# Optimization experiments

Hardware: AMD Instinct MI355X
Metric: run time of the kernel (lower is better)

Reference implementation:

```python
import jax, jax.numpy as jnp
import numpy as np
from jax import lax

# channels holding diagonal entries of the embedded 4x4 bA (16:32) and bW (32:48)
_DIAG_CH = np.array([16, 21, 26, 31, 32, 37, 42, 47])
_EPS = 1e-4  # Tikhonov term for per-pixel matrix inversion stability


def _interp_matrix(out_n, in_n):
    """Dense 1D bicubic (a=-0.75) align_corners=True interpolation matrix, torch-compatible."""
    if out_n == in_n:
        return jnp.eye(out_n, dtype=jnp.float32)
    a = -0.75
    scale = (in_n - 1) / (out_n - 1)
    src = np.arange(out_n) * scale
    i0 = np.floor(src).astype(np.int64)
    W = np.zeros((out_n, in_n), np.float64)
    rows = np.arange(out_n)
    for k in range(-1, 3):
        t = np.abs(src - (i0 + k))
        w = np.where(t <= 1.0, (a + 2) * t**3 - (a + 3) * t**2 + 1.0,
                     np.where(t < 2.0, a * t**3 - 5 * a * t**2 + 8 * a * t - 4 * a, 0.0))
        np.add.at(W, (rows, np.clip(i0 + k, 0, in_n - 1)), w)  # border replication
    return jnp.asarray(W, jnp.float32)


def _conv(x, w, b):
    y = lax.conv_general_dilated(x, w, (1, 1), 'SAME',
                                 dimension_numbers=('NCHW', 'OIHW', 'NCHW'))
    return y + b[None, :, None, None]


def _leaky(x):
    return jnp.where(x >= 0, x, 0.01 * x)


def _mm_features(x):
    """compute_mm + intensity: x is (b,48,h,w) -> (b,17,h,w)."""
    b, c, h, w = x.shape
    v = jnp.moveaxis(x, 1, -1)                 # (b,h,w,48)
    F = v[..., :16].reshape(b, h, w, 4, 4)     # intensity frames
    A = v[..., 16:32].reshape(b, h, w, 4, 4)   # analyzer calib bA
    Wm = v[..., 32:48].reshape(b, h, w, 4, 4)  # generator calib bW
    eye = _EPS * jnp.eye(4, dtype=x.dtype)
    M = jnp.linalg.inv(A + eye) @ F @ jnp.linalg.inv(Wm + eye)  # M = A^-1 F W^-1
    inten = v[..., :16].mean(-1)[:, None]      # (b,1,h,w)
    m = jnp.moveaxis(M.reshape(b, h, w, 16), -1, 1)  # (b,16,h,w)
    return jnp.concatenate([inten, m], axis=1)


def _maxpool4(x):
    b, c, h, w = x.shape
    return x.reshape(b, c, h // 4, 4, w // 4, 4).max(axis=(3, 5))


def setup_inputs() -> dict:
    key = jax.random.key(0)
    ks = jax.random.split(key, 6)
    x = 0.3 * jax.random.normal(ks[0], (2, 48, 512, 512), jnp.float32)
    diag = jnp.asarray(_DIAG_CH)
    x = x.at[:, diag].add(1.0)  # well-conditioned per-pixel bA/bW ~ I + noise

    def bias48():
        return jnp.zeros((48,), jnp.float32).at[diag].set(1.0)

    iW0 = 0.05 * jax.random.normal(ks[1], (48, 48, 3, 3), jnp.float32)
    iW1 = 0.05 * jax.random.normal(ks[2], (48, 48, 3, 3), jnp.float32)
    oW0 = 0.05 * jax.random.normal(ks[3], (17, 17, 3, 3), jnp.float32)
    oW1 = 0.05 * jax.random.normal(ks[4], (17, 17, 3, 3), jnp.float32)
    return dict(x=x,
                iW0=iW0, iB0=bias48(), iW1=iW1, iB1=bias48(),
                oW0=oW0, oB0=jnp.zeros((17,), jnp.float32),
                oW1=oW1, oB1=jnp.zeros((17,), jnp.float32))


def reference(x, iW0, iB0, iW1, iB1, oW0, oB0, oW1, oB1):
    b, _, h, w = x.shape
    iparams = [(iW0, iB0), (iW1, iB1)]
    oparams = [(oW0, oB0), (oW1, oB1)]
    outs = []
    for lvl in range(2):  # fixed pyramid levels
        x = _leaky(_conv(x, *iparams[lvl]))
        m = _mm_features(x)                       # (b,17,hl,wl)
        Wh = _interp_matrix(h, m.shape[2])
        Ww = _interp_matrix(w, m.shape[3])
        m = jnp.einsum('Oh,bchw->bcOw', Wh, m)    # bicubic upsample rows
        m = jnp.einsum('Pw,bchw->bchP', Ww, m)    # bicubic upsample cols
        m = _leaky(_conv(m, *oparams[lvl]))
        outs.append(m)
        x = _maxpool4(x)
    return jnp.concatenate(outs, axis=1)          # (b,34,h,w)
```

## Files before the change

### kernel.cpp

```cpp
#include <hip/hip_runtime.h>
#include <math.h>


__device__ __forceinline__ float leakyf(float t) { return t >= 0.0f ? t : 0.01f * t; }

template<int CIN, int OCPT, int PX, int TW, bool DO_POOL, bool TWO_SRC>
__global__ __launch_bounds__(256, 2)
void conv3x3_leaky(const float* __restrict__ in, const float* __restrict__ wgt,
                   const float* __restrict__ bias, float* __restrict__ out,
                   float* __restrict__ pool_out,
                   int H, int W, int COUT, int NG,
                   int in_bstride, int out_bstride, int out_coff,
                   const float* __restrict__ in2, const float* __restrict__ wgt2,
                   const float* __restrict__ bias2, int coff2, int z_split)
{
    constexpr int XG     = TW / PX;
    constexpr int TH     = 256 / XG;
    constexpr int COLS   = TW + 2;
    constexpr int ROWS   = TH + 2;
    constexpr int STRIDE = (COLS + 3) & ~3;
    constexpr int TSZ    = ROWS * STRIDE;
    constexpr int ELEMS  = ROWS * COLS;
    constexpr int K      = (ELEMS + 255) / 256;
    constexpr int NV     = PX + 2;

    __shared__ float tile[2 * TSZ];
    __shared__ float wlds[CIN * OCPT * 12];
    __shared__ float blds[OCPT];

    const float* insel = in;
    const float* wsel  = wgt;
    const float* bsel  = bias;
    int coff = out_coff;
    int bz   = blockIdx.z;
    if (TWO_SRC && bz >= z_split) {
        bz -= z_split;
        insel = in2; wsel = wgt2; bsel = bias2; coff = coff2;
    }

    const int tid   = threadIdx.x;
    const int tx    = tid & (XG - 1);
    const int ty    = tid / XG;
    const int g     = bz % NG;
    const int b     = bz / NG;
    const int obase = g * OCPT;
    const int row0  = blockIdx.y * TH;
    const int col0  = blockIdx.x * TW;
    const int HW    = H * W;

    for (int idx = tid; idx < CIN * OCPT * 9; idx += 256) {
        int c  = idx / (OCPT * 9);
        int r2 = idx - c * (OCPT * 9);
        int o  = r2 / 9;
        int k2 = r2 - o * 9;
        int og = obase + o;
        wlds[(c * OCPT + o) * 12 + k2] = (og < COUT) ? wsel[(og * CIN + c) * 9 + k2] : 0.0f;
    }
    if (tid < OCPT) {
        int og = obase + tid;
        blds[tid] = (og < COUT) ? bsel[og] : 0.0f;
    }

    int goff[K], loff[K];
#pragma unroll
    for (int k = 0; k < K; ++k) {
        int idx = tid + k * 256;
        if (idx < ELEMS) {
            int r  = idx / COLS;
            int cc = idx - r * COLS;
            int gr = row0 - 1 + r;
            int gc = col0 - 1 + cc;
            bool v = (gr >= 0 && gr < H && gc >= 0 && gc < W);
            goff[k] = v ? (gr * W + gc) : -1;
            loff[k] = r * STRIDE + cc;
        } else {
            goff[k] = -1;
            loff[k] = -1;
        }
    }

    const float* inb = insel + (size_t)b * in_bstride;

    float sreg[K];
    {
        const float* ic = inb;
#pragma unroll
        for (int k = 0; k < K; ++k) {
            float v = 0.0f;
            if (goff[k] >= 0) v = ic[goff[k]];
            sreg[k] = v;
        }
#pragma unroll
        for (int k = 0; k < K; ++k)
            if (loff[k] >= 0) tile[loff[k]] = sreg[k];
    }
    __syncthreads();

    float acc[OCPT][PX];
#pragma unroll
    for (int o = 0; o < OCPT; ++o)
#pragma unroll
        for (int p = 0; p < PX; ++p) acc[o][p] = 0.0f;

    for (int c = 0; c < CIN; ++c) {
        if (c + 1 < CIN) {
            const float* ic = inb + (c + 1) * HW;
#pragma unroll
            for (int k = 0; k < K; ++k) {
                float v = 0.0f;
                if (goff[k] >= 0) v = ic[goff[k]];
                sreg[k] = v;
            }
        }

        {
            const float* tb = &tile[(c & 1) * TSZ];
            float v[3][NV];
#pragma unroll
            for (int rr = 0; rr < 3; ++rr) {
                const float* tp = tb + (ty + rr) * STRIDE + tx * PX;
                float4 a0 = *(const float4*)tp;
                v[rr][0] = a0.x; v[rr][1] = a0.y; v[rr][2] = a0.z; v[rr][3] = a0.w;
                if constexpr (PX == 8) {
                    float4 a1 = *(const float4*)(tp + 4);
                    float2 a2 = *(const float2*)(tp + 8);
                    v[rr][4] = a1.x; v[rr][5] = a1.y; v[rr][6] = a1.z; v[rr][7] = a1.w;
                    v[rr][8] = a2.x; v[rr][9] = a2.y;
                } else {
                    float2 a1 = *(const float2*)(tp + 4);
                    v[rr][4] = a1.x; v[rr][5] = a1.y;
                }
            }
#pragma unroll
            for (int o = 0; o < OCPT; ++o) {
                const float* wp = &wlds[(c * OCPT + o) * 12];
                float4 w0 = *(const float4*)wp;
                float4 w1 = *(const float4*)(wp + 4);
                float w8 = wp[8];
                float wk[9] = {w0.x, w0.y, w0.z, w0.w, w1.x, w1.y, w1.z, w1.w, w8};
#pragma unroll
                for (int px = 0; px < PX; ++px) {
                    float s = acc[o][px];
#pragma unroll
                    for (int kr = 0; kr < 3; ++kr)
#pragma unroll
                        for (int kc = 0; kc < 3; ++kc)
                            s = fmaf(wk[kr * 3 + kc], v[kr][px + kc], s);
                    acc[o][px] = s;
                }
            }
        }

        if (c + 1 < CIN) {
            float* tb = &tile[((c + 1) & 1) * TSZ];
#pragma unroll
            for (int k = 0; k < K; ++k)
                if (loff[k] >= 0) tb[loff[k]] = sreg[k];
            __syncthreads();
        }
    }

    const int orow = row0 + ty;
    float* outb = out + (size_t)b * out_bstride;
#pragma unroll
    for (int o = 0; o < OCPT; ++o) {
        int og = obase + o;
        if (og < COUT) {
            float bv = blds[o];
            float r[PX];
#pragma unroll
            for (int p = 0; p < PX; ++p) { float t = acc[o][p] + bv; r[p] = leakyf(t); }
            float* op = outb + ((coff + og) * H + orow) * W + col0 + tx * PX;
#pragma unroll
            for (int q = 0; q < PX / 4; ++q)
                *(float4*)(op + 4 * q) = make_float4(r[4*q], r[4*q+1], r[4*q+2], r[4*q+3]);
        }
    }

    if constexpr (DO_POOL) {
        static_assert(PX == 8 && XG == 8, "pool fusion assumes PX=8, XG=8");
        const int pH = H >> 2, pW = W >> 2;
        const int prow = (row0 + ty) >> 2;
        const int pcol = (col0 >> 2) + tx * 2;
        const bool writer = (ty & 3) == 0;
#pragma unroll
        for (int o = 0; o < OCPT; ++o) {
            float bv = blds[o];
            float c0 = leakyf(acc[o][0] + bv);
            c0 = fmaxf(c0, leakyf(acc[o][1] + bv));
            c0 = fmaxf(c0, leakyf(acc[o][2] + bv));
            c0 = fmaxf(c0, leakyf(acc[o][3] + bv));
            float c1 = leakyf(acc[o][4] + bv);
            c1 = fmaxf(c1, leakyf(acc[o][5] + bv));
            c1 = fmaxf(c1, leakyf(acc[o][6] + bv));
            c1 = fmaxf(c1, leakyf(acc[o][7] + bv));
            c0 = fmaxf(c0, __shfl_xor(c0, 8));
            c0 = fmaxf(c0, __shfl_xor(c0, 16));
            c1 = fmaxf(c1, __shfl_xor(c1, 8));
            c1 = fmaxf(c1, __shfl_xor(c1, 16));
            if (writer) {
                int og = obase + o;
                *(float2*)(pool_out + ((size_t)(b * COUT + og) * pH + prow) * pW + pcol)
                    = make_float2(c0, c1);
            }
        }
    }
}

__device__ __forceinline__ void inv4x4(const double* m, double* invOut)
{
    double inv[16];
    inv[0]  =  m[5]*m[10]*m[15] - m[5]*m[11]*m[14] - m[9]*m[6]*m[15] + m[9]*m[7]*m[14] + m[13]*m[6]*m[11] - m[13]*m[7]*m[10];
    inv[4]  = -m[4]*m[10]*m[15] + m[4]*m[11]*m[14] + m[8]*m[6]*m[15] - m[8]*m[7]*m[14] - m[12]*m[6]*m[11] + m[12]*m[7]*m[10];
    inv[8]  =  m[4]*m[9]*m[15]  - m[4]*m[11]*m[13] - m[8]*m[5]*m[15] + m[8]*m[7]*m[13] + m[12]*m[5]*m[11] - m[12]*m[7]*m[9];
    inv[12] = -m[4]*m[9]*m[14]  + m[4]*m[10]*m[13] + m[8]*m[5]*m[14] - m[8]*m[6]*m[13] - m[12]*m[5]*m[10] + m[12]*m[6]*m[9];
    inv[1]  = -m[1]*m[10]*m[15] + m[1]*m[11]*m[14] + m[9]*m[2]*m[15] - m[9]*m[3]*m[14] - m[13]*m[2]*m[11] + m[13]*m[3]*m[10];
    inv[5]  =  m[0]*m[10]*m[15] - m[0]*m[11]*m[14] - m[8]*m[2]*m[15] + m[8]*m[3]*m[14] + m[12]*m[2]*m[11] - m[12]*m[3]*m[10];
    inv[9]  = -m[0]*m[9]*m[15]  + m[0]*m[11]*m[13] + m[8]*m[1]*m[15] - m[8]*m[3]*m[13] - m[12]*m[1]*m[11] + m[12]*m[3]*m[9];
    inv[13] =  m[0]*m[9]*m[14]  - m[0]*m[10]*m[13] - m[8]*m[1]*m[14] + m[8]*m[2]*m[13] + m[12]*m[1]*m[10] - m[12]*m[2]*m[9];
    inv[2]  =  m[1]*m[6]*m[15]  - m[1]*m[7]*m[14]  - m[5]*m[2]*m[15] + m[5]*m[3]*m[14] + m[13]*m[2]*m[7]  - m[13]*m[3]*m[6];
    inv[6]  = -m[0]*m[6]*m[15]  + m[0]*m[7]*m[14]  + m[4]*m[2]*m[15] - m[4]*m[3]*m[14] - m[12]*m[2]*m[7]  + m[12]*m[3]*m[6];
    inv[10] =  m[0]*m[5]*m[15]  - m[0]*m[7]*m[13]  - m[4]*m[1]*m[15] + m[4]*m[3]*m[13] + m[12]*m[1]*m[7]  - m[12]*m[3]*m[5];
    inv[14] = -m[0]*m[5]*m[14]  + m[0]*m[6]*m[13]  + m[4]*m[1]*m[14] - m[4]*m[2]*m[13] - m[12]*m[1]*m[6]  + m[12]*m[2]*m[5];
    inv[3]  = -m[1]*m[6]*m[11]  + m[1]*m[7]*m[10]  + m[5]*m[2]*m[11] - m[5]*m[3]*m[10] - m[9]*m[2]*m[7]   + m[9]*m[3]*m[6];
    inv[7]  =  m[0]*m[6]*m[11]  - m[0]*m[7]*m[10]  - m[4]*m[2]*m[11] + m[4]*m[3]*m[10] + m[8]*m[2]*m[7]   - m[8]*m[3]*m[6];
    inv[11] = -m[0]*m[5]*m[11]  + m[0]*m[7]*m[9]   + m[4]*m[1]*m[11] - m[4]*m[3]*m[9]  - m[8]*m[1]*m[7]   + m[8]*m[3]*m[5];
    inv[15] =  m[0]*m[5]*m[10]  - m[0]*m[6]*m[9]   - m[4]*m[1]*m[10] + m[4]*m[2]*m[9]  + m[8]*m[1]*m[6]   - m[8]*m[2]*m[5];
    double det = m[0]*inv[0] + m[1]*inv[4] + m[2]*inv[8] + m[3]*inv[12];
    det = 1.0 / det;
#pragma unroll
    for (int i = 0; i < 16; ++i) invOut[i] = inv[i] * det;
}

__device__ __forceinline__ void matmul4(const double* A, const double* B, double* C)
{
#pragma unroll
    for (int r = 0; r < 4; ++r)
#pragma unroll
        for (int c = 0; c < 4; ++c) {
            double s = 0.0;
#pragma unroll
            for (int k = 0; k < 4; ++k) s += A[r * 4 + k] * B[k * 4 + c];
            C[r * 4 + c] = s;
        }
}

__global__ __launch_bounds__(256)
void mm_features_kernel(const float* __restrict__ y0, float* __restrict__ m0,
                        int HW0, int n0,
                        const float* __restrict__ y1, float* __restrict__ m1,
                        int HW1, int ntot)
{
    int p = blockIdx.x * 256 + threadIdx.x;
    if (p >= ntot) return;
    const float* y; float* mo; int HW;
    if (p < n0) { y = y0; mo = m0; HW = HW0; }
    else        { p -= n0; y = y1; mo = m1; HW = HW1; }
    int b  = p / HW;
    int sp = p - b * HW;
    const float* base = y + (size_t)b * 48 * HW + sp;

    double A[16];
#pragma unroll
    for (int i = 0; i < 16; ++i) {
        double e = (i == 0 || i == 5 || i == 10 || i == 15) ? 1e-4 : 0.0;
        A[i] = (double)base[(16 + i) * HW] + e;
    }
    double iA[16];
    inv4x4(A, iA);

    double F[16];
    double s = 0.0;
#pragma unroll
    for (int i = 0; i < 16; ++i) { F[i] = (double)base[i * HW]; }
#pragma unroll
    for (int i = 0; i < 16; ++i) s += F[i];
    s *= (1.0 / 16.0);

    double T[16];
    matmul4(iA, F, T);

    double Wm[16];
#pragma unroll
    for (int i = 0; i < 16; ++i) {
        double e = (i == 0 || i == 5 || i == 10 || i == 15) ? 1e-4 : 0.0;
        Wm[i] = (double)base[(32 + i) * HW] + e;
    }
    double iW[16];
    inv4x4(Wm, iW);

    double M[16];
    matmul4(T, iW, M);

    float* ob = mo + (size_t)b * 17 * HW + sp;
    ob[0] = (float)s;
#pragma unroll
    for (int i = 0; i < 16; ++i) ob[(1 + i) * HW] = (float)M[i];
}

__device__ __forceinline__ float cubwf(float t)
{
    t = fabsf(t);
    if (t <= 1.0f) return (1.25f * t - 2.25f) * t * t + 1.0f;
    if (t < 2.0f)  return (((t - 5.0f) * t + 8.0f) * t - 4.0f) * -0.75f;
    return 0.0f;
}

__global__ __launch_bounds__(256)
void bicubic_up4_kernel(const float* __restrict__ src, float* __restrict__ dst, int n)
{
    int idx = blockIdx.x * 256 + threadIdx.x;
    if (idx >= n) return;
    int P  = idx & 511;
    int O  = (idx >> 9) & 511;
    int bc = idx >> 18;
    const float scale = 127.0f / 511.0f;
    float sh = O * scale, sw = P * scale;
    int i0 = (int)floorf(sh), j0 = (int)floorf(sw);
    float wh[4], ww[4];
#pragma unroll
    for (int k = 0; k < 4; ++k) {
        wh[k] = cubwf(sh - (float)(i0 + k - 1));
        ww[k] = cubwf(sw - (float)(j0 + k - 1));
    }
    const float* sp = src + bc * 16384;
    float acc = 0.0f;
#pragma unroll
    for (int ki = 0; ki < 4; ++ki) {
        int ih = min(max(i0 - 1 + ki, 0), 127);
        float rs = 0.0f;
#pragma unroll
        for (int kj = 0; kj < 4; ++kj) {
            int iw = min(max(j0 - 1 + kj, 0), 127);
            rs = fmaf(ww[kj], sp[ih * 128 + iw], rs);
        }
        acc = fmaf(wh[ki], rs, acc);
    }
    dst[idx] = acc;
}

extern "C" void kernel_launch(void* const* d_in, const int* in_sizes, int n_in,
                              void* d_out, int out_size, void* d_ws, size_t ws_size,
                              hipStream_t stream)
{
    const float* x   = (const float*)d_in[0];
    const float* iW0 = (const float*)d_in[1];
    const float* iB0 = (const float*)d_in[2];
    const float* iW1 = (const float*)d_in[3];
    const float* iB1 = (const float*)d_in[4];
    const float* oW0 = (const float*)d_in[5];
    const float* oB0 = (const float*)d_in[6];
    const float* oW1 = (const float*)d_in[7];
    const float* oB1 = (const float*)d_in[8];
    float* out = (float*)d_out;
    float* ws  = (float*)d_ws;

    float* y0 = ws;
    float* m0 = ws + 25165824;
    float* x1 = ws + 34078720;
    float* y1 = ws + 35651584;
    float* m1 = ws + 37224448;
    float* u  = ws;

    conv3x3_leaky<48, 8, 8, 64, true, false><<<dim3(8, 16, 12), 256, 0, stream>>>(
        x, iW0, iB0, y0, x1, 512, 512, 48, 6, 48 * 512 * 512, 48 * 512 * 512, 0,
        nullptr, nullptr, nullptr, 0, 0);

    conv3x3_leaky<48, 4, 4, 32, false, false><<<dim3(4, 4, 24), 256, 0, stream>>>(
        x1, iW1, iB1, y1, nullptr, 128, 128, 48, 12, 48 * 128 * 128, 48 * 128 * 128, 0,
        nullptr, nullptr, nullptr, 0, 0);

    mm_features_kernel<<<(2 * 512 * 512 + 2 * 128 * 128) / 256, 256, 0, stream>>>(
        y0, m0, 512 * 512, 2 * 512 * 512, y1, m1, 128 * 128,
        2 * 512 * 512 + 2 * 128 * 128);

    bicubic_up4_kernel<<<(2 * 17 * 512 * 512) / 256, 256, 0, stream>>>(m1, u, 2 * 17 * 512 * 512);

    conv3x3_leaky<17, 9, 8, 64, false, true><<<dim3(8, 16, 8), 256, 0, stream>>>(
        m0, oW0, oB0, out, nullptr, 512, 512, 17, 2, 17 * 512 * 512, 34 * 512 * 512, 0,
        u, oW1, oB1, 17, 4);
}
```

Measured before the change: 632.5 us.

## Stage conv input tiles directly into LDS with global_load_lds

Replaces the register-staged double-buffered tile loads (global to registers, then registers to LDS) with direct global-to-LDS loads via __builtin_amdgcn_global_load_lds. Each wave copies whole tile rows with per-lane column masks. Out-of-bounds halo cells are zeroed once in both buffers up front. This cuts register pressure and the VALU/LDS store traffic of staging. The risk is that the plain __syncthreads may not wait for the asynchronous LDS writes to finish (vmcnt), and that the 4-byte per-lane loads are less efficient than before.

Result: slower. 697.3 us (+10.2%).

```diff
diff --git a/kernel.cpp b/kernel.cpp
--- a/kernel.cpp
+++ b/kernel.cpp
@@ -3,6 +3,31 @@
 
 
 __device__ __forceinline__ float leakyf(float t) { return t >= 0.0f ? t : 0.01f * t; }
+
+__device__ __forceinline__ void gload_lds4(const float* g, float* l)
+{
+    __builtin_amdgcn_global_load_lds(
+        (const __attribute__((address_space(1))) void*)g,
+        (__attribute__((address_space(3))) void*)l, 4, 0, 0);
+}
+
+#define STAGE_CH(BUF)                                                         \
+    {                                                                         \
+        sbase += HW;                                                          \
+        float* buf_ = (BUF);                                                  \
+        _Pragma("unroll")                                                     \
+        for (int i_ = 0; i_ < RPW; ++i_) {                                    \
+            if (rvmask & (1u << i_)) {                                        \
+                const float* rp_ = sbase + (size_t)(wv + 4 * i_) * W;         \
+                _Pragma("unroll")                                             \
+                for (int cb_ = 0; cb_ < COLS; cb_ += 64) {                    \
+                    if (cok[cb_ / 64])                                        \
+                        gload_lds4(rp_ + cb_ + lane,                          \
+                                   &buf_[(wv + 4 * i_) * STRIDE + cb_]);      \
+                }                                                             \
+            }                                                                 \
+        }                                                                     \
+    }
 
 template<int CIN, int OCPT, int PX, int TW, bool DO_POOL, bool TWO_SRC>
 __global__ __launch_bounds__(256, 2)
@@ -21,8 +46,8 @@
     constexpr int STRIDE = (COLS + 3) & ~3;
     constexpr int TSZ    = ROWS * STRIDE;
     constexpr int ELEMS  = ROWS * COLS;
-    constexpr int K      = (ELEMS + 255) / 256;
     constexpr int NV     = PX + 2;
+    constexpr int RPW    = (ROWS + 3) / 4;
 
     __shared__ float tile[2 * TSZ];
     __shared__ float wlds[CIN * OCPT * 12];
@@ -39,6 +64,8 @@
     }
 
     const int tid   = threadIdx.x;
+    const int lane  = tid & 63;
+    const int wv    = tid >> 6;
     const int tx    = tid & (XG - 1);
     const int ty    = tid / XG;
     const int g     = bz % NG;
@@ -61,39 +88,35 @@
         blds[tid] = (og < COUT) ? bsel[og] : 0.0f;
     }
 
-    int goff[K], loff[K];
-#pragma unroll
-    for (int k = 0; k < K; ++k) {
-        int idx = tid + k * 256;
-        if (idx < ELEMS) {
-            int r  = idx / COLS;
-            int cc = idx - r * COLS;
-            int gr = row0 - 1 + r;
-            int gc = col0 - 1 + cc;
-            bool v = (gr >= 0 && gr < H && gc >= 0 && gc < W);
-            goff[k] = v ? (gr * W + gc) : -1;
-            loff[k] = r * STRIDE + cc;
-        } else {
-            goff[k] = -1;
-            loff[k] = -1;
-        }
-    }
-
+    for (int idx = tid; idx < ELEMS; idx += 256) {
+        int r  = idx / COLS;
+        int cc = idx - r * COLS;
+        int gr = row0 - 1 + r;
+        int gc = col0 - 1 + cc;
+        if (!(gr >= 0 && gr < H && gc >= 0 && gc < W)) {
+            tile[r * STRIDE + cc] = 0.0f;
+            tile[TSZ + r * STRIDE + cc] = 0.0f;
+        }
+    }
+
+    bool cok[(COLS + 63) / 64];
+#pragma unroll
+    for (int j = 0; j < (COLS + 63) / 64; ++j) {
+        int cc = j * 64 + lane;
+        int gc = col0 - 1 + cc;
+        cok[j] = (cc < COLS) && (gc >= 0) && (gc < W);
+    }
+    unsigned rvmask = 0;
+#pragma unroll
+    for (int i = 0; i < RPW; ++i) {
+        int r  = wv + 4 * i;
+        int gr = row0 - 1 + r;
+        if (r < ROWS && gr >= 0 && gr < H) rvmask |= (1u << i);
+    }
     const float* inb = insel + (size_t)b * in_bstride;
-
-    float sreg[K];
-    {
-        const float* ic = inb;
-#pragma unroll
-        for (int k = 0; k < K; ++k) {
-            float v = 0.0f;
-            if (goff[k] >= 0) v = ic[goff[k]];
-            sreg[k] = v;
-        }
-#pragma unroll
-        for (int k = 0; k < K; ++k)
-            if (loff[k] >= 0) tile[loff[k]] = sreg[k];
-    }
+    const float* sbase = inb + (size_t)(row0 - 1) * W + (col0 - 1) - HW;
+
+    STAGE_CH(&tile[0]);
     __syncthreads();
 
     float acc[OCPT][PX];
@@ -103,15 +126,7 @@
         for (int p = 0; p < PX; ++p) acc[o][p] = 0.0f;
 
     for (int c = 0; c < CIN; ++c) {
-        if (c + 1 < CIN) {
-            const float* ic = inb + (c + 1) * HW;
-#pragma unroll
-            for (int k = 0; k < K; ++k) {
-                float v = 0.0f;
-                if (goff[k] >= 0) v = ic[goff[k]];
-                sreg[k] = v;
-            }
-        }
+        if (c + 1 < CIN) STAGE_CH(&tile[((c + 1) & 1) * TSZ]);
 
         {
             const float* tb = &tile[(c & 1) * TSZ];
@@ -151,13 +166,7 @@
             }
         }
 
-        if (c + 1 < CIN) {
-            float* tb = &tile[((c + 1) & 1) * TSZ];
-#pragma unroll
-            for (int k = 0; k < K; ++k)
-                if (loff[k] >= 0) tb[loff[k]] = sreg[k];
-            __syncthreads();
-        }
+        if (c + 1 < CIN) __syncthreads();
     }
 
     const int orow = row0 + ty;
@@ -207,6 +216,8 @@
     }
 }
 
+#undef STAGE_CH
+
 __device__ __forceinline__ void inv4x4(const double* m, double* invOut)
 {
     double inv[16];
```
